# Kernel optimization log

Measured on AMD Instinct MI355X. Metric: run time of the kernel, lower is better.

## Reference

```python
import jax, jax.numpy as jnp
import numpy as np
from jax import lax

EPS = 1e-6
K1D = 3  # DACA conv1d kernel size for C=64


def binquant(x):
    # forward of BinaryQuantize_Quad (sign); STE only matters for bwd
    return jnp.sign(x)


def daca(x, w1d):
    # x: [B,C,H,W] -> per-channel sigmoid gate [B,C,1,1]
    b, c, h, w = x.shape
    flat = x.reshape(b, c, h * w)
    ch_mean = flat.mean(axis=2)
    ch_var = flat.var(axis=2, ddof=1) + EPS  # torch.var default unbiased=True
    ch_std = jnp.sqrt(ch_var)
    ch_abs = jnp.abs(flat).mean(axis=2)  # adaptive avg pool of |x|
    y = jnp.stack([ch_abs, ch_mean, ch_std], axis=1)  # [B,3,C]
    y = lax.conv_general_dilated(
        y, w1d, window_strides=(1,), padding=[(K1D // 2, K1D // 2)],
        dimension_numbers=("NCH", "OIH", "NCH"))  # [B,1,C]
    return jax.nn.sigmoid(y[:, 0, :, None, None])  # [B,C,1,1]


def hard_binary_conv(x, w):
    # scaling: mean |w| over (in,kh,kw), per out-channel, detached
    scale = jnp.mean(jnp.abs(w), axis=(1, 2, 3), keepdims=True)
    cw = jnp.clip(w, -1.0, 1.0)
    bw = lax.stop_gradient(scale * jnp.sign(w) - cw) + cw  # value=scale*sign(w), grad via clip
    return lax.conv_general_dilated(
        x, bw, window_strides=(1, 1), padding=[(1, 1), (1, 1)],
        dimension_numbers=("NCHW", "OIHW", "NCHW"))


def rprelu(x, b0, a, b1):
    y = x + b0
    y = jnp.where(y > 0, y, a[None, :, None, None] * y)  # PReLU per-channel
    return y + b1


def setup_inputs() -> dict:
    key = jax.random.key(0)
    ks = jax.random.split(key, 7)
    C = 64
    x = jax.random.normal(ks[0], (8, C, 256, 256), dtype=jnp.float32)
    w_conv = jax.random.normal(ks[1], (C, C, 3, 3), dtype=jnp.float32) * 0.1
    w1d = jax.random.normal(ks[2], (1, 3, K1D), dtype=jnp.float32) * 0.3
    b_move = jax.random.normal(ks[3], (1, C, 1, 1), dtype=jnp.float32) * 0.02
    pr_b0 = jax.random.normal(ks[4], (1, C, 1, 1), dtype=jnp.float32) * 0.02
    prelu_a = jnp.full((C,), 0.25, dtype=jnp.float32)
    pr_b1 = jax.random.normal(ks[5], (1, C, 1, 1), dtype=jnp.float32) * 0.02
    return {"x": x, "b_move": b_move, "w_conv": w_conv, "w1d": w1d,
            "pr_b0": pr_b0, "prelu_a": prelu_a, "pr_b1": pr_b1}


def reference(x, b_move, w_conv, w1d, pr_b0, prelu_a, pr_b1):
    out = x + b_move                 # LearnableBias move0
    scale = daca(out, w1d)           # [B,C,1,1] gate
    out = binquant(out)              # sign binarization of activations
    out = hard_binary_conv(out, w_conv)
    out = out * scale
    out = rprelu(out, pr_b0, prelu_a, pr_b1)
    return out + x                   # residual
```

## Files before the change

kernel.cpp:

```cpp
#include <hip/hip_runtime.h>
#include <stdint.h>

#define BB 8
#define C  64
#define H  256
#define W  256
#define HW (H*W)
#define EPSV 1e-6f

__global__ __launch_bounds__(256) void k_pack_stats(
    const float* __restrict__ x,
    const float* __restrict__ bmove,
    unsigned long long* __restrict__ packed,
    float* __restrict__ part ) {
  int blk = blockIdx.x;
  int b   = blk >> 7;
  int rg  = blk & 127;
  int h0  = rg << 1;
  int tid = threadIdx.x;
  int wid = tid >> 6, lane = tid & 63;

  __shared__ float4 lds4[64 * 33];
  __shared__ float fred[4][3][64];

  float bm = bmove[lane];
  float s = 0.f, s2 = 0.f, sa = 0.f;

  int p4l = tid & 31;
  int cg  = tid >> 5;
  const size_t bbase = (size_t)b * C * HW;

  for (int tile = 0; tile < 4; ++tile) {
    int h  = h0 + (tile >> 1);
    int wb = (tile & 1) << 7;
    __syncthreads();
    #pragma unroll
    for (int cc = 0; cc < 8; ++cc) {
      int c = cg + (cc << 3);
      const float4* src = (const float4*)(x + bbase + (size_t)c * HW + h * W + wb) + p4l;
      lds4[c * 33 + p4l] = *src;
    }
    __syncthreads();
    unsigned long long* pdst = packed + ((size_t)(b * H + h)) * W + wb;
    #pragma unroll
    for (int k = 0; k < 8; ++k) {
      int p4i = (wid << 3) + k;
      float4 v = lds4[lane * 33 + p4i];
      float a0 = v.x + bm, a1 = v.y + bm, a2 = v.z + bm, a3 = v.w + bm;
      s  += a0 + a1 + a2 + a3;
      s2 += a0*a0 + a1*a1 + a2*a2 + a3*a3;
      sa += fabsf(a0) + fabsf(a1) + fabsf(a2) + fabsf(a3);
      unsigned long long q0 = __ballot(a0 > 0.f);
      unsigned long long q1 = __ballot(a1 > 0.f);
      unsigned long long q2 = __ballot(a2 > 0.f);
      unsigned long long q3 = __ballot(a3 > 0.f);
      unsigned long long qq = (lane == 0) ? q0 : (lane == 1) ? q1
                            : (lane == 2) ? q2 : q3;
      if (lane < 4) pdst[(p4i << 2) + lane] = qq;
    }
  }
  fred[wid][0][lane] = s;
  fred[wid][1][lane] = s2;
  fred[wid][2][lane] = sa;
  __syncthreads();
  if (tid < 192) {
    int st = tid >> 6, c = tid & 63;
    float v = fred[0][st][c] + fred[1][st][c] + fred[2][st][c] + fred[3][st][c];
    part[((size_t)(b * 64 + c) * 3 + st) * 128 + rg] = v;
  }
}

__global__ __launch_bounds__(512) void k_gate(
    const float* __restrict__ part,
    const float* __restrict__ w_conv,
    const float* __restrict__ w1d,
    float* __restrict__ alpha,
    unsigned long long* __restrict__ wsign) {
  __shared__ float stA[512], stM[512], stS[512];
  __shared__ float swv[64];
  int tid = threadIdx.x;
  {
    const float4* p = (const float4*)(part + (size_t)tid * 384);
    float s = 0.f, s2 = 0.f, sa = 0.f;
    for (int k = 0;  k < 32; k++) { float4 v = p[k]; s  += v.x + v.y + v.z + v.w; }
    for (int k = 32; k < 64; k++) { float4 v = p[k]; s2 += v.x + v.y + v.z + v.w; }
    for (int k = 64; k < 96; k++) { float4 v = p[k]; sa += v.x + v.y + v.z + v.w; }
    const float invN = 1.f / (float)HW;
    float mean = s * invN;
    float var  = (s2 - s * s * invN) * (1.f / (float)(HW - 1)) + EPSV;
    stA[tid] = sa * invN;
    stM[tid] = mean;
    stS[tid] = sqrtf(var);
  }
  {
    int o = tid >> 3, g = tid & 7;
    const float* wo = w_conv + o * 576 + g * 72;
    float s = 0.f;
    unsigned long long wb[9] = {0,0,0,0,0,0,0,0,0};
    #pragma unroll
    for (int i = 0; i < 8; i++) {
      #pragma unroll
      for (int t = 0; t < 9; t++) {
        float v = wo[i * 9 + t];
        s += fabsf(v);
        if (v > 0.f) wb[t] |= (1ull << (g * 8 + i));
      }
    }
    #pragma unroll
    for (int off = 4; off > 0; off >>= 1) {
      s += __shfl_down(s, off, 8);
      #pragma unroll
      for (int t = 0; t < 9; t++)
        wb[t] |= __shfl_down(wb[t], off, 8);
    }
    if (g == 0) {
      swv[o] = s * (1.f / 576.f);
      #pragma unroll
      for (int t = 0; t < 9; t++) wsign[o * 9 + t] = wb[t];
    }
  }
  __syncthreads();
  int b = tid >> 6, c = tid & 63;
  float y = 0.f;
  #pragma unroll
  for (int k = 0; k < 3; k++) {
    int cc = c + k - 1;
    if (cc >= 0 && cc < 64) {
      int j = b * 64 + cc;
      y += stA[j] * w1d[0 * 3 + k] + stM[j] * w1d[1 * 3 + k] + stS[j] * w1d[2 * 3 + k];
    }
  }
  float gate = 1.f / (1.f + expf(-y));
  alpha[tid] = gate * swv[c];
}

__global__ __launch_bounds__(256) void k_conv(const unsigned long long* __restrict__ packed,
                                              const unsigned long long* __restrict__ wsign,
                                              const float* __restrict__ alpha,
                                              const float* __restrict__ x,
                                              const float* __restrict__ pr_b0,
                                              const float* __restrict__ prelu_a,
                                              const float* __restrict__ pr_b1,
                                              float* __restrict__ out) {
  int bh = blockIdx.x;
  int b = bh >> 8, h = bh & 255;
  int w = threadIdx.x;
  __shared__ unsigned long long rows[3][W];
  bool r0v = (h > 0), r2v = (h < H - 1);
  const unsigned long long* pb = packed + (size_t)b * HW;
  rows[1][w] = pb[h * W + w];
  if (r0v) rows[0][w] = pb[(h - 1) * W + w];
  if (r2v) rows[2][w] = pb[(h + 1) * W + w];
  __syncthreads();

  bool lv = (w > 0), rv = (w < W - 1);
  unsigned long long vmL = lv ? ~0ull : 0ull;
  unsigned long long vmR = rv ? ~0ull : 0ull;
  unsigned long long nL[3], nC[3], nR[3];
  #pragma unroll
  for (int r = 0; r < 3; r++) {
    nC[r] = rows[r][w];
    nL[r] = rows[r][lv ? w - 1 : w];
    nR[r] = rows[r][rv ? w + 1 : w];
  }
  int nrows = 1 + (int)r0v + (int)r2v;
  int ncols = 1 + (int)lv + (int)rv;
  float base = 64.f * (float)(nrows * ncols);
  size_t xoff = (size_t)b * C * HW + h * W + w;

  for (int o = 0; o < 64; o++) {
    const unsigned long long* wso = wsign + o * 9;
    int cnt = 0;
    if (r0v) {
      cnt += __popcll((nL[0] ^ wso[0]) & vmL);
      cnt += __popcll( nC[0] ^ wso[1]);
      cnt += __popcll((nR[0] ^ wso[2]) & vmR);
    }
    cnt += __popcll((nL[1] ^ wso[3]) & vmL);
    cnt += __popcll( nC[1] ^ wso[4]);
    cnt += __popcll((nR[1] ^ wso[5]) & vmR);
    if (r2v) {
      cnt += __popcll((nL[2] ^ wso[6]) & vmL);
      cnt += __popcll( nC[2] ^ wso[7]);
      cnt += __popcll((nR[2] ^ wso[8]) & vmR);
    }
    float dot = base - 2.f * (float)cnt;
    float v = dot * alpha[b * 64 + o];
    float y = v + pr_b0[o];
    y = (y > 0.f) ? y : prelu_a[o] * y;
    y += pr_b1[o];
    size_t idx = xoff + (size_t)o * HW;
    __builtin_nontemporal_store(y + x[idx], &out[idx]);
  }
}

extern "C" void kernel_launch(void* const* d_in, const int* in_sizes, int n_in,
                              void* d_out, int out_size, void* d_ws, size_t ws_size,
                              hipStream_t stream) {
  const float* x       = (const float*)d_in[0];
  const float* b_move  = (const float*)d_in[1];
  const float* w_conv  = (const float*)d_in[2];
  const float* w1d     = (const float*)d_in[3];
  const float* pr_b0   = (const float*)d_in[4];
  const float* prelu_a = (const float*)d_in[5];
  const float* pr_b1   = (const float*)d_in[6];
  float* out = (float*)d_out;

  char* ws = (char*)d_ws;
  unsigned long long* packed = (unsigned long long*)ws;
  float* part  = (float*)(ws + 4194304);
  float* alpha = (float*)(ws + 4194304 + 786432);
  unsigned long long* wsign = (unsigned long long*)(ws + 4194304 + 786432 + 2048);

  k_pack_stats<<<1024, 256, 0, stream>>>(x, b_move, packed, part);
  k_gate<<<1, 512, 0, stream>>>(part, w_conv, w1d, alpha, wsign);
  k_conv<<<BB * H, 256, 0, stream>>>(packed, wsign, alpha, x,
                                     pr_b0, prelu_a, pr_b1, out);
}
```

Before: 128.7 us.

## Split stats from packing and compute four output pixels per thread in conv

Statistics move into their own per-(b,c) reduction kernel, so the pack kernel only produces sign bits and the gate kernel reads final sums instead of partials. The conv kernel now handles four rows per block and four adjacent pixels per thread. It reuses the neighbouring packed words across pixels and uses float4 loads and stores for x and out. The cost is reading x twice, once for stats and once for packing, plus an extra launch, in exchange for fewer LDS/weight reloads and wider memory accesses in the conv.

```diff
diff --git a/kernel.cpp b/kernel.cpp
--- a/kernel.cpp
+++ b/kernel.cpp
@@ -8,24 +8,55 @@
 #define HW (H*W)
 #define EPSV 1e-6f
 
-__global__ __launch_bounds__(256) void k_pack_stats(
-    const float* __restrict__ x,
-    const float* __restrict__ bmove,
-    unsigned long long* __restrict__ packed,
-    float* __restrict__ part ) {
+typedef unsigned long long u64;
+typedef float __attribute__((ext_vector_type(4))) f32x4;
+
+__global__ __launch_bounds__(256) void k_stats(const float* __restrict__ x,
+                                               const float* __restrict__ bmove,
+                                               float* __restrict__ sums ) {
+  int bc = blockIdx.x;
+  float bm = bmove[bc & 63];
+  const f32x4* p = (const f32x4*)(x + (size_t)bc * HW);
+  int t = threadIdx.x;
+  float s = 0.f, s2 = 0.f, sa = 0.f;
+  #pragma unroll 8
+  for (int k = 0; k < 64; ++k) {
+    f32x4 v = p[(k << 8) | t];
+    float a0 = v.x + bm, a1 = v.y + bm, a2 = v.z + bm, a3 = v.w + bm;
+    s  += a0 + a1 + a2 + a3;
+    s2 += a0*a0 + a1*a1 + a2*a2 + a3*a3;
+    sa += fabsf(a0) + fabsf(a1) + fabsf(a2) + fabsf(a3);
+  }
+  #pragma unroll
+  for (int off = 32; off > 0; off >>= 1) {
+    s  += __shfl_down(s,  off, 64);
+    s2 += __shfl_down(s2, off, 64);
+    sa += __shfl_down(sa, off, 64);
+  }
+  __shared__ float red[4][3];
+  int wid = t >> 6;
+  if ((t & 63) == 0) { red[wid][0] = s; red[wid][1] = s2; red[wid][2] = sa; }
+  __syncthreads();
+  if (t == 0) {
+    float S  = red[0][0] + red[1][0] + red[2][0] + red[3][0];
+    float S2 = red[0][1] + red[1][1] + red[2][1] + red[3][1];
+    float SA = red[0][2] + red[1][2] + red[2][2] + red[3][2];
+    sums[bc] = S; sums[512 + bc] = S2; sums[1024 + bc] = SA;
+  }
+}
+
+__global__ __launch_bounds__(256) void k_pack(const float* __restrict__ x,
+                                              const float* __restrict__ bmove,
+                                              u64* __restrict__ packed) {
   int blk = blockIdx.x;
   int b   = blk >> 7;
   int rg  = blk & 127;
   int h0  = rg << 1;
   int tid = threadIdx.x;
   int wid = tid >> 6, lane = tid & 63;
-
-  __shared__ float4 lds4[64 * 33];
-  __shared__ float fred[4][3][64];
+  __shared__ f32x4 lds4[64 * 33];
 
   float bm = bmove[lane];
-  float s = 0.f, s2 = 0.f, sa = 0.f;
-
   int p4l = tid & 31;
   int cg  = tid >> 5;
   const size_t bbase = (size_t)b * C * HW;
@@ -37,54 +68,37 @@
     #pragma unroll
     for (int cc = 0; cc < 8; ++cc) {
       int c = cg + (cc << 3);
-      const float4* src = (const float4*)(x + bbase + (size_t)c * HW + h * W + wb) + p4l;
-      lds4[c * 33 + p4l] = *src;
+      lds4[c * 33 + p4l] =
+          *((const f32x4*)(x + bbase + (size_t)c * HW + h * W + wb) + p4l);
     }
     __syncthreads();
-    unsigned long long* pdst = packed + ((size_t)(b * H + h)) * W + wb;
+    u64* pdst = packed + ((size_t)(b * H + h)) * W + wb;
     #pragma unroll
     for (int k = 0; k < 8; ++k) {
       int p4i = (wid << 3) + k;
-      float4 v = lds4[lane * 33 + p4i];
-      float a0 = v.x + bm, a1 = v.y + bm, a2 = v.z + bm, a3 = v.w + bm;
-      s  += a0 + a1 + a2 + a3;
-      s2 += a0*a0 + a1*a1 + a2*a2 + a3*a3;
-      sa += fabsf(a0) + fabsf(a1) + fabsf(a2) + fabsf(a3);
-      unsigned long long q0 = __ballot(a0 > 0.f);
-      unsigned long long q1 = __ballot(a1 > 0.f);
-      unsigned long long q2 = __ballot(a2 > 0.f);
-      unsigned long long q3 = __ballot(a3 > 0.f);
-      unsigned long long qq = (lane == 0) ? q0 : (lane == 1) ? q1
-                            : (lane == 2) ? q2 : q3;
+      f32x4 v = lds4[lane * 33 + p4i];
+      u64 q0 = __ballot(v.x + bm > 0.f);
+      u64 q1 = __ballot(v.y + bm > 0.f);
+      u64 q2 = __ballot(v.z + bm > 0.f);
+      u64 q3 = __ballot(v.w + bm > 0.f);
+      u64 qa = (lane & 1) ? q1 : q0;
+      u64 qb = (lane & 1) ? q3 : q2;
+      u64 qq = (lane & 2) ? qb : qa;
       if (lane < 4) pdst[(p4i << 2) + lane] = qq;
     }
   }
-  fred[wid][0][lane] = s;
-  fred[wid][1][lane] = s2;
-  fred[wid][2][lane] = sa;
-  __syncthreads();
-  if (tid < 192) {
-    int st = tid >> 6, c = tid & 63;
-    float v = fred[0][st][c] + fred[1][st][c] + fred[2][st][c] + fred[3][st][c];
-    part[((size_t)(b * 64 + c) * 3 + st) * 128 + rg] = v;
-  }
-}
-
-__global__ __launch_bounds__(512) void k_gate(
-    const float* __restrict__ part,
-    const float* __restrict__ w_conv,
-    const float* __restrict__ w1d,
-    float* __restrict__ alpha,
-    unsigned long long* __restrict__ wsign) {
+}
+
+__global__ __launch_bounds__(512) void k_gate(const float* __restrict__ sums,
+                                              const float* __restrict__ w_conv,
+                                              const float* __restrict__ w1d,
+                                              float* __restrict__ alpha,
+                                              u64* __restrict__ wsign) {
   __shared__ float stA[512], stM[512], stS[512];
   __shared__ float swv[64];
   int tid = threadIdx.x;
   {
-    const float4* p = (const float4*)(part + (size_t)tid * 384);
-    float s = 0.f, s2 = 0.f, sa = 0.f;
-    for (int k = 0;  k < 32; k++) { float4 v = p[k]; s  += v.x + v.y + v.z + v.w; }
-    for (int k = 32; k < 64; k++) { float4 v = p[k]; s2 += v.x + v.y + v.z + v.w; }
-    for (int k = 64; k < 96; k++) { float4 v = p[k]; sa += v.x + v.y + v.z + v.w; }
+    float s = sums[tid], s2 = sums[512 + tid], sa = sums[1024 + tid];
     const float invN = 1.f / (float)HW;
     float mean = s * invN;
     float var  = (s2 - s * s * invN) * (1.f / (float)(HW - 1)) + EPSV;
@@ -96,27 +110,27 @@
     int o = tid >> 3, g = tid & 7;
     const float* wo = w_conv + o * 576 + g * 72;
     float s = 0.f;
-    unsigned long long wb[9] = {0,0,0,0,0,0,0,0,0};
+    u64 wb[9] = {0,0,0,0,0,0,0,0,0};
     #pragma unroll
     for (int i = 0; i < 8; i++) {
       #pragma unroll
-      for (int t = 0; t < 9; t++) {
-        float v = wo[i * 9 + t];
+      for (int tp = 0; tp < 9; tp++) {
+        float v = wo[i * 9 + tp];
         s += fabsf(v);
-        if (v > 0.f) wb[t] |= (1ull << (g * 8 + i));
+        if (v > 0.f) wb[tp] |= (1ull << (g * 8 + i));
       }
     }
     #pragma unroll
     for (int off = 4; off > 0; off >>= 1) {
       s += __shfl_down(s, off, 8);
       #pragma unroll
-      for (int t = 0; t < 9; t++)
-        wb[t] |= __shfl_down(wb[t], off, 8);
+      for (int tp = 0; tp < 9; tp++)
+        wb[tp] |= __shfl_down(wb[tp], off, 8);
     }
     if (g == 0) {
       swv[o] = s * (1.f / 576.f);
       #pragma unroll
-      for (int t = 0; t < 9; t++) wsign[o * 9 + t] = wb[t];
+      for (int tp = 0; tp < 9; tp++) wsign[o * 9 + tp] = wb[tp];
     }
   }
   __syncthreads();
@@ -134,63 +148,92 @@
   alpha[tid] = gate * swv[c];
 }
 
-__global__ __launch_bounds__(256) void k_conv(const unsigned long long* __restrict__ packed,
-                                              const unsigned long long* __restrict__ wsign,
-                                              const float* __restrict__ alpha,
-                                              const float* __restrict__ x,
-                                              const float* __restrict__ pr_b0,
-                                              const float* __restrict__ prelu_a,
-                                              const float* __restrict__ pr_b1,
-                                              float* __restrict__ out) {
-  int bh = blockIdx.x;
-  int b = bh >> 8, h = bh & 255;
-  int w = threadIdx.x;
-  __shared__ unsigned long long rows[3][W];
-  bool r0v = (h > 0), r2v = (h < H - 1);
-  const unsigned long long* pb = packed + (size_t)b * HW;
-  rows[1][w] = pb[h * W + w];
-  if (r0v) rows[0][w] = pb[(h - 1) * W + w];
-  if (r2v) rows[2][w] = pb[(h + 1) * W + w];
+__global__ __launch_bounds__(256) void k_conv4(const u64* __restrict__ packed,
+                                               const u64* __restrict__ wsign,
+                                               const float* __restrict__ alpha,
+                                               const float* __restrict__ x,
+                                               const float* __restrict__ pr_b0,
+                                               const float* __restrict__ prelu_a,
+                                               const float* __restrict__ pr_b1,
+                                               float* __restrict__ out) {
+  int blk = blockIdx.x;
+  int b = blk >> 6, hg = blk & 63;
+  int h0 = hg << 2;
+  int t = threadIdx.x;
+  __shared__ u64 rows[6][W];
+  const u64* pb = packed + (size_t)b * H * W;
+  #pragma unroll
+  for (int r = 0; r < 6; ++r) {
+    int hr = h0 - 1 + r;
+    rows[r][t] = (hr >= 0 && hr < H) ? pb[hr * W + t] : 0ull;
+  }
   __syncthreads();
 
-  bool lv = (w > 0), rv = (w < W - 1);
-  unsigned long long vmL = lv ? ~0ull : 0ull;
-  unsigned long long vmR = rv ? ~0ull : 0ull;
-  unsigned long long nL[3], nC[3], nR[3];
-  #pragma unroll
-  for (int r = 0; r < 3; r++) {
-    nC[r] = rows[r][w];
-    nL[r] = rows[r][lv ? w - 1 : w];
-    nR[r] = rows[r][rv ? w + 1 : w];
-  }
-  int nrows = 1 + (int)r0v + (int)r2v;
-  int ncols = 1 + (int)lv + (int)rv;
-  float base = 64.f * (float)(nrows * ncols);
-  size_t xoff = (size_t)b * C * HW + h * W + w;
-
-  for (int o = 0; o < 64; o++) {
-    const unsigned long long* wso = wsign + o * 9;
-    int cnt = 0;
-    if (r0v) {
-      cnt += __popcll((nL[0] ^ wso[0]) & vmL);
-      cnt += __popcll( nC[0] ^ wso[1]);
-      cnt += __popcll((nR[0] ^ wso[2]) & vmR);
-    }
-    cnt += __popcll((nL[1] ^ wso[3]) & vmL);
-    cnt += __popcll( nC[1] ^ wso[4]);
-    cnt += __popcll((nR[1] ^ wso[5]) & vmR);
-    if (r2v) {
-      cnt += __popcll((nL[2] ^ wso[6]) & vmL);
-      cnt += __popcll( nC[2] ^ wso[7]);
-      cnt += __popcll((nR[2] ^ wso[8]) & vmR);
-    }
-    float dot = base - 2.f * (float)cnt;
-    float v = dot * alpha[b * 64 + o];
-    float y = v + pr_b0[o];
-    y = (y > 0.f) ? y : prelu_a[o] * y;
-    y += pr_b1[o];
-    size_t idx = xoff + (size_t)o * HW;
-    __builtin_nontemporal_store(y + x[idx], &out[idx]);
+  int tr = t >> 6, lane = t & 63;
+  int tw = lane << 2;
+  int h  = h0 + tr;
+  bool rTop = (h > 0), rBot = (h < H - 1);
+  u64 vm0 = (lane == 0)  ? 0ull : ~0ull;
+  u64 vm5 = (lane == 63) ? 0ull : ~0ull;
+
+  u64 nw[3][6];
+  #pragma unroll
+  for (int rr = 0; rr < 3; ++rr) {
+    #pragma unroll
+    for (int j = 0; j < 6; ++j) {
+      int wi = tw - 1 + j;
+      wi = (wi < 0) ? 0 : (wi > W - 1 ? W - 1 : wi);
+      nw[rr][j] = rows[tr + rr][wi];
+    }
+  }
+  int nr = 1 + (int)rTop + (int)rBot;
+  float base0 = 64.f * (float)nr * ((lane == 0)  ? 2.f : 3.f);
+  float base1 = 64.f * (float)nr * 3.f;
+  float base3 = 64.f * (float)nr * ((lane == 63) ? 2.f : 3.f);
+
+  size_t xoff = (size_t)b * C * HW + (size_t)h * W + tw;
+  const float* al = alpha + b * 64;
+
+  for (int o = 0; o < 64; ++o) {
+    const u64* ws = wsign + o * 9;
+    u64 w0=ws[0], w1=ws[1], w2=ws[2], w3=ws[3], w4=ws[4],
+        w5=ws[5], w6=ws[6], w7=ws[7], w8=ws[8];
+    int c0 = 0, c1 = 0, c2 = 0, c3 = 0;
+    if (rTop) {
+      c0 += __popcll((nw[0][0]^w0)&vm0) + __popcll(nw[0][1]^w1) + __popcll(nw[0][2]^w2);
+      c1 += __popcll(nw[0][1]^w0) + __popcll(nw[0][2]^w1) + __popcll(nw[0][3]^w2);
+      c2 += __popcll(nw[0][2]^w0) + __popcll(nw[0][3]^w1) + __popcll(nw[0][4]^w2);
+      c3 += __popcll(nw[0][3]^w0) + __popcll(nw[0][4]^w1) + __popcll((nw[0][5]^w2)&vm5);
+    }
+    {
+      c0 += __popcll((nw[1][0]^w3)&vm0) + __popcll(nw[1][1]^w4) + __popcll(nw[1][2]^w5);
+      c1 += __popcll(nw[1][1]^w3) + __popcll(nw[1][2]^w4) + __popcll(nw[1][3]^w5);
+      c2 += __popcll(nw[1][2]^w3) + __popcll(nw[1][3]^w4) + __popcll(nw[1][4]^w5);
+      c3 += __popcll(nw[1][3]^w3) + __popcll(nw[1][4]^w4) + __popcll((nw[1][5]^w5)&vm5);
+    }
+    if (rBot) {
+      c0 += __popcll((nw[2][0]^w6)&vm0) + __popcll(nw[2][1]^w7) + __popcll(nw[2][2]^w8);
+      c1 += __popcll(nw[2][1]^w6) + __popcll(nw[2][2]^w7) + __popcll(nw[2][3]^w8);
+      c2 += __popcll(nw[2][2]^w6) + __popcll(nw[2][3]^w7) + __popcll(nw[2][4]^w8);
+      c3 += __popcll(nw[2][3]^w6) + __popcll(nw[2][4]^w7) + __popcll((nw[2][5]^w8)&vm5);
+    }
+    float a  = al[o];
+    float b0 = pr_b0[o], pa = prelu_a[o], b1 = pr_b1[o];
+    f32x4 xr = *(const f32x4*)(x + xoff + (size_t)o * HW);
+    float d0 = (base0 - 2.f*(float)c0) * a + b0;
+    float d1 = (base1 - 2.f*(float)c1) * a + b0;
+    float d2 = (base1 - 2.f*(float)c2) * a + b0;
+    float d3 = (base3 - 2.f*(float)c3) * a + b0;
+    d0 = (d0 > 0.f) ? d0 : pa * d0;
+    d1 = (d1 > 0.f) ? d1 : pa * d1;
+    d2 = (d2 > 0.f) ? d2 : pa * d2;
+    d3 = (d3 > 0.f) ? d3 : pa * d3;
+    f32x4 ov;
+    ov.x = d0 + b1 + xr.x;
+    ov.y = d1 + b1 + xr.y;
+    ov.z = d2 + b1 + xr.z;
+    ov.w = d3 + b1 + xr.w;
+    __builtin_nontemporal_store(ov, (f32x4*)(out + xoff + (size_t)o * HW));
   }
 }
 
@@ -207,13 +250,14 @@
   float* out = (float*)d_out;
 
   char* ws = (char*)d_ws;
-  unsigned long long* packed = (unsigned long long*)ws;
-  float* part  = (float*)(ws + 4194304);
-  float* alpha = (float*)(ws + 4194304 + 786432);
-  unsigned long long* wsign = (unsigned long long*)(ws + 4194304 + 786432 + 2048);
-
-  k_pack_stats<<<1024, 256, 0, stream>>>(x, b_move, packed, part);
-  k_gate<<<1, 512, 0, stream>>>(part, w_conv, w1d, alpha, wsign);
-  k_conv<<<BB * H, 256, 0, stream>>>(packed, wsign, alpha, x,
-                                     pr_b0, prelu_a, pr_b1, out);
-}
+  u64*   packed = (u64*)ws;
+  float* sums   = (float*)(ws + 4194304);
+  float* alpha  = (float*)(ws + 4194304 + 8192);
+  u64*   wsign  = (u64*)(ws + 4194304 + 16384);
+
+  k_stats<<<512, 256, 0, stream>>>(x, b_move, sums);
+  k_pack<<<1024, 256, 0, stream>>>(x, b_move, packed);
+  k_gate<<<1, 512, 0, stream>>>(sums, w_conv, w1d, alpha, wsign);
+  k_conv4<<<512, 256, 0, stream>>>(packed, wsign, alpha, x,
+                                   pr_b0, prelu_a, pr_b1, out);
+}
```

Result: faster. 120.5 us (-6.4%).
